# Performance work log

Measured on AMD Instinct MI355X. Metric: run time of the kernel, lower is better.

Reference implementation:

```python
import jax, jax.numpy as jnp
import numpy as np

B, L, H, HKV, D, HID, FFN = 32, 4096, 32, 2, 128, 4096, 13696
ROT = 64  # rotary_dim = kv_channels // 2 (GLM style)
EPS = 1e-5


def setup_inputs() -> dict:
    key = jax.random.key(0)
    ks = jax.random.split(key, 9)
    s = 0.02
    return {
        "hidden_states": jax.random.normal(ks[0], (B, HID), jnp.float32),
        "context_lens": jax.random.randint(ks[1], (B,), 1, L - 1, dtype=jnp.int32),
        "key_cache": jax.random.normal(ks[2], (B, L, HKV, D), jnp.float32),
        "value_cache": jax.random.normal(ks[3], (B, L, HKV, D), jnp.float32),
        "w_ln1": jnp.ones((HID,), jnp.float32),
        "w_ln2": jnp.ones((HID,), jnp.float32),
        "w_qkv": jax.random.normal(ks[4], (HID, H * D + 2 * HKV * D), jnp.float32) * s,
        "b_qkv": jax.random.normal(ks[5], (H * D + 2 * HKV * D,), jnp.float32) * s,
        "w_dense": jax.random.normal(ks[6], (H * D, HID), jnp.float32) * s,
        "w_h4h": jax.random.normal(ks[7], (HID, 2 * FFN), jnp.float32) * s,
        "w_4hh": jax.random.normal(ks[8], (FFN, HID), jnp.float32) * s,
    }


def rmsnorm(x, w):
    v = jnp.mean(x.astype(jnp.float32) ** 2, axis=-1, keepdims=True)
    return (w * (x * jax.lax.rsqrt(v + EPS))).astype(x.dtype)


def apply_rope(x, pos):
    # x: [B, heads, D]; GPT-J interleaved rotary on first ROT dims (glm=True)
    half = ROT // 2
    inv = 1.0 / (10000.0 ** (jnp.arange(half, dtype=jnp.float32) / half))
    f = pos.astype(jnp.float32)[:, None] * inv[None, :]          # [B, half]
    cos, sin = jnp.cos(f)[:, None, :], jnp.sin(f)[:, None, :]    # [B,1,half]
    xr, xp = x[..., :ROT], x[..., ROT:]
    x1, x2 = xr[..., 0::2], xr[..., 1::2]
    rot = jnp.stack([x1 * cos - x2 * sin, x2 * cos + x1 * sin], axis=-1).reshape(xr.shape)
    return jnp.concatenate([rot, xp], axis=-1)


def reference(hidden_states, context_lens, key_cache, value_cache,
              w_ln1, w_ln2, w_qkv, b_qkv, w_dense, w_h4h, w_4hh):
    # input RMSNorm
    ln1 = rmsnorm(hidden_states, w_ln1)
    # fused QKV projection (add_qkv_bias=True)
    qkv = ln1 @ w_qkv + b_qkv
    q, k, v = jnp.split(qkv, [H * D, H * D + HKV * D], axis=-1)
    q = apply_rope(q.reshape(B, H, D), context_lens)
    k = apply_rope(k.reshape(B, HKV, D), context_lens)
    v = v.reshape(B, HKV, D)
    # write new K/V into the paged cache at this token's slot
    kc = key_cache.at[jnp.arange(B), context_lens].set(k)
    vc = value_cache.at[jnp.arange(B), context_lens].set(v)
    # GQA attention: 32 q heads grouped over 2 kv heads
    qg = q.reshape(B, HKV, H // HKV, D)
    scores = jnp.einsum('bghd,blgd->bghl', qg, kc) * (D ** -0.5)
    mask = jnp.arange(L)[None, :] <= context_lens[:, None]       # [B, L]
    scores = jnp.where(mask[:, None, None, :], scores, -jnp.inf)
    p = jax.nn.softmax(scores, axis=-1)
    ctx = jnp.einsum('bghl,blgd->bghd', p, vc).reshape(B, H * D)
    attn_out = ctx @ w_dense                                     # add_bias_linear=False
    x = hidden_states + attn_out                                  # residual pre-LN
    ln2 = rmsnorm(x, w_ln2)
    g, u = jnp.split(ln2 @ w_h4h, 2, axis=-1)
    out = (jax.nn.silu(g) * u) @ w_4hh + x
    return out
```

## Files before the change

kernel.cpp:

```cpp
#include <hip/hip_runtime.h>
#include <hip/hip_bf16.h>

#define B_    32
#define L_    4096
#define H_    32
#define HKV_  2
#define GQ_   16
#define D_    128
#define HID_  4096
#define FFN_  13696
#define NQKV_ 4608
#define ROT_  64
#define EPS_  1e-5f

#define WAVE_POS_ 128
#define NSPLIT_   32

typedef __attribute__((ext_vector_type(8))) __bf16 bf16x8;
typedef __attribute__((ext_vector_type(4))) float  f32x4;

__global__ __launch_bounds__(256) void rmsnorm1_k(const float* __restrict__ x,
                                                  const float* __restrict__ w,
                                                  __bf16* __restrict__ out)
{
    int b = blockIdx.x;
    const float* row = x + (size_t)b * HID_;
    float vals[16];
    float ss = 0.f;
#pragma unroll
    for (int i = 0; i < 16; ++i) {
        vals[i] = row[threadIdx.x + i * 256];
        ss += vals[i] * vals[i];
    }
#pragma unroll
    for (int m = 1; m < 64; m <<= 1) ss += __shfl_xor(ss, m);
    __shared__ float wred[4];
    if ((threadIdx.x & 63) == 0) wred[threadIdx.x >> 6] = ss;
    __syncthreads();
    ss = wred[0] + wred[1] + wred[2] + wred[3];
    float rs = rsqrtf(ss / HID_ + EPS_);
#pragma unroll
    for (int i = 0; i < 16; ++i) {
        int idx = threadIdx.x + i * 256;
        out[(size_t)b * HID_ + idx] = (__bf16)(w[idx] * vals[i] * rs);
    }
}

template<int K, int N, int KSPLIT>
__global__ __launch_bounds__(256) void gemm16(const __bf16* __restrict__ A,
                                              const float* __restrict__ W,
                                              float* __restrict__ Cp)
{
    static_assert(K % 32 == 0, "K");
    constexpr int ksteps = K / 32;
    constexpr int nch    = KSPLIT * 4;
    const int lane = threadIdx.x & 63;
    const int wid  = threadIdx.x >> 6;
    const int n0   = blockIdx.x * 32;
    const int r    = lane & 15;
    const int g4   = lane >> 4;
    const int cid  = blockIdx.y * 4 + wid;
    const int s0   = (ksteps * cid) / nch;
    const int s1   = (ksteps * (cid + 1)) / nch;

    const int kk_b = lane >> 3;
    const int c4   = (lane & 7) * 4;

    __shared__ __bf16 tiles[4][32][40];
    __bf16 (*tile)[40] = tiles[wid];

    f32x4 acc00 = {0.f,0.f,0.f,0.f}, acc01 = acc00, acc10 = acc00, acc11 = acc00;
    const __bf16* a0p = A + (size_t)r * K;
    const __bf16* a1p = A + (size_t)(r + 16) * K;

    float4 pf[4];
    auto issue = [&](int s) {
        const float* wk = W + (size_t)(s * 32 + kk_b) * N + n0 + c4;
#pragma unroll
        for (int it = 0; it < 4; ++it)
            pf[it] = *(const float4*)(wk + (size_t)(it * 8) * N);
    };

    if (s0 < s1) issue(s0);
    for (int s = s0; s < s1; ++s) {
        float4 cur[4];
#pragma unroll
        for (int it = 0; it < 4; ++it) cur[it] = pf[it];
        if (s + 1 < s1) issue(s + 1);
#pragma unroll
        for (int it = 0; it < 4; ++it) {
            int kk = it * 8 + kk_b;
            tile[c4 + 0][kk] = (__bf16)cur[it].x;
            tile[c4 + 1][kk] = (__bf16)cur[it].y;
            tile[c4 + 2][kk] = (__bf16)cur[it].z;
            tile[c4 + 3][kk] = (__bf16)cur[it].w;
        }
        asm volatile("s_waitcnt lgkmcnt(0)" ::: "memory");
        __builtin_amdgcn_sched_barrier(0);
        bf16x8 b0  = *(const bf16x8*)&tile[r][g4 * 8];
        bf16x8 b1  = *(const bf16x8*)&tile[r + 16][g4 * 8];
        bf16x8 av0 = *(const bf16x8*)(a0p + s * 32 + g4 * 8);
        bf16x8 av1 = *(const bf16x8*)(a1p + s * 32 + g4 * 8);
        acc00 = __builtin_amdgcn_mfma_f32_16x16x32_bf16(av0, b0, acc00, 0, 0, 0);
        acc10 = __builtin_amdgcn_mfma_f32_16x16x32_bf16(av1, b0, acc10, 0, 0, 0);
        acc01 = __builtin_amdgcn_mfma_f32_16x16x32_bf16(av0, b1, acc01, 0, 0, 0);
        acc11 = __builtin_amdgcn_mfma_f32_16x16x32_bf16(av1, b1, acc11, 0, 0, 0);
        asm volatile("s_waitcnt lgkmcnt(0)" ::: "memory");
        __builtin_amdgcn_sched_barrier(0);
    }

    __shared__ float red[4][32][32];
#pragma unroll
    for (int i = 0; i < 4; ++i) {
        red[wid][g4 * 4 + i][r]           = acc00[i];
        red[wid][g4 * 4 + i][16 + r]      = acc01[i];
        red[wid][16 + g4 * 4 + i][r]      = acc10[i];
        red[wid][16 + g4 * 4 + i][16 + r] = acc11[i];
    }
    __syncthreads();
    for (int idx = threadIdx.x; idx < 1024; idx += 256) {
        int row = idx >> 5, col = idx & 31;
        float v = red[0][row][col] + red[1][row][col] + red[2][row][col] + red[3][row][col];
        Cp[((size_t)blockIdx.y * 32 + row) * N + n0 + col] = v;
    }
}

__global__ __launch_bounds__(256) void qkv_epi_k(const float* __restrict__ part,
                                                 const float* __restrict__ bias,
                                                 const int* __restrict__ ctxl,
                                                 __bf16* __restrict__ qbf,
                                                 float* __restrict__ knew,
                                                 float* __restrict__ vnew)
{
    __shared__ float rowv[NQKV_];
    __shared__ float cs[32], sn[32];
    int b = blockIdx.x;
    int pos = ctxl[b];
    if (threadIdx.x < 32) {
        int t = threadIdx.x;
        float inv = powf(10000.f, -(float)t * (1.0f / 32.0f));
        float f = (float)pos * inv;
        float sv, cv; sincosf(f, &sv, &cv);
        cs[t] = cv; sn[t] = sv;
    }
    for (int i = threadIdx.x; i < NQKV_; i += 256) {
        float v = bias[i];
#pragma unroll
        for (int p = 0; p < 4; ++p) v += part[((size_t)p * B_ + b) * NQKV_ + i];
        rowv[i] = v;
    }
    __syncthreads();
    const float qscale = 0.08838834764831845f;
    for (int i = threadIdx.x; i < HID_; i += 256) {
        int d = i & 127;
        float o;
        if (d < ROT_) {
            int t = d >> 1;
            float cv = cs[t], sv = sn[t];
            float x1 = rowv[i & ~1], x2 = rowv[i | 1];
            o = (d & 1) ? (x2 * cv + x1 * sv) : (x1 * cv - x2 * sv);
        } else o = rowv[i];
        qbf[(size_t)b * HID_ + i] = (__bf16)(o * qscale);
    }
    for (int i = threadIdx.x; i < HKV_ * D_; i += 256) {
        int d = i & 127;
        float o;
        if (d < ROT_) {
            int t = d >> 1;
            float cv = cs[t], sv = sn[t];
            float x1 = rowv[HID_ + (i & ~1)], x2 = rowv[HID_ + (i | 1)];
            o = (d & 1) ? (x2 * cv + x1 * sv) : (x1 * cv - x2 * sv);
        } else o = rowv[HID_ + i];
        knew[(size_t)b * HKV_ * D_ + i] = o;
        vnew[(size_t)b * HKV_ * D_ + i] = rowv[HID_ + HKV_ * D_ + i];
    }
}

__global__ __launch_bounds__(256) void attn_k(const float* __restrict__ kc,
                                              const float* __restrict__ vc,
                                              const float* __restrict__ knew,
                                              const float* __restrict__ vnew,
                                              const __bf16* __restrict__ qbf,
                                              const int* __restrict__ ctxl,
                                              float* __restrict__ part)
{
    const int bg  = blockIdx.x;
    const int b   = bg >> 1, g = bg & 1;
    const int wid = threadIdx.x >> 6;
    const int split = blockIdx.y * 4 + wid;
    const int ctx = ctxl[b];
    const int p0  = split * WAVE_POS_;
    __shared__ __bf16 plds_all[4][16][40];
    if (p0 > ctx) return;
    const int pend = min(p0 + WAVE_POS_ - 1, ctx);
    const int lane = threadIdx.x & 63;
    const int r = lane & 15, g4 = lane >> 4;

    bf16x8 qf[4];
    {
        const __bf16* qp = qbf + (size_t)b * HID_ + (g * GQ_ + r) * D_ + g4 * 8;
#pragma unroll
        for (int kk = 0; kk < 4; ++kk) qf[kk] = *(const bf16x8*)(qp + kk * 32);
    }
    f32x4 acc[8];
#pragma unroll
    for (int dt = 0; dt < 8; ++dt) acc[dt] = (f32x4){0.f,0.f,0.f,0.f};
    float m_run[4], l_run[4];
#pragma unroll
    for (int i = 0; i < 4; ++i) { m_run[i] = -1e30f; l_run[i] = 0.f; }

    auto plds = plds_all[wid];
    const float* kbase = kc + ((size_t)b * L_ * HKV_ + g) * D_;
    const float* vbase = vc + ((size_t)b * L_ * HKV_ + g) * D_;
    const float* knp = knew + (size_t)(b * HKV_ + g) * D_;
    const float* vnp = vnew + (size_t)(b * HKV_ + g) * D_;

    for (int pc = p0; pc <= pend; pc += 32) {
        f32x4 sf[2];
#pragma unroll
        for (int pt = 0; pt < 2; ++pt) {
            int pos = pc + pt * 16 + r;
            const float* krow = (pos == ctx) ? knp : kbase + (size_t)pos * (HKV_ * D_);
            f32x4 s = {0.f,0.f,0.f,0.f};
#pragma unroll
            for (int kk = 0; kk < 4; ++kk) {
                const float4* kp = (const float4*)(krow + kk * 32 + g4 * 8);
                float4 fa = kp[0], fb = kp[1];
                bf16x8 kf = { (__bf16)fa.x, (__bf16)fa.y, (__bf16)fa.z, (__bf16)fa.w,
                              (__bf16)fb.x, (__bf16)fb.y, (__bf16)fb.z, (__bf16)fb.w };
                s = __builtin_amdgcn_mfma_f32_16x16x32_bf16(qf[kk], kf, s, 0, 0, 0);
            }
            sf[pt] = s;
        }
#pragma unroll
        for (int pt = 0; pt < 2; ++pt) {
            int pos = pc + pt * 16 + r;
            if (pos > ctx) {
#pragma unroll
                for (int i = 0; i < 4; ++i) sf[pt][i] = -1e30f;
            }
        }
#pragma unroll
        for (int i = 0; i < 4; ++i) {
            float mv = fmaxf(sf[0][i], sf[1][i]);
            mv = fmaxf(mv, __shfl_xor(mv, 1));
            mv = fmaxf(mv, __shfl_xor(mv, 2));
            mv = fmaxf(mv, __shfl_xor(mv, 4));
            mv = fmaxf(mv, __shfl_xor(mv, 8));
            float mnew = fmaxf(m_run[i], mv);
            float sc = __expf(m_run[i] - mnew);
            l_run[i] *= sc;
            m_run[i] = mnew;
#pragma unroll
            for (int dt = 0; dt < 8; ++dt) acc[dt][i] *= sc;
        }
#pragma unroll
        for (int pt = 0; pt < 2; ++pt) {
#pragma unroll
            for (int i = 0; i < 4; ++i) {
                float e = __expf(sf[pt][i] - m_run[i]);
                l_run[i] += e;
                plds[g4 * 4 + i][pt * 16 + r] = (__bf16)e;
            }
        }
        asm volatile("s_waitcnt lgkmcnt(0)" ::: "memory");
        __builtin_amdgcn_sched_barrier(0);
        bf16x8 pa = *(const bf16x8*)&plds[r][g4 * 8];
        const float* vrows[8];
#pragma unroll
        for (int j = 0; j < 8; ++j) {
            int pos = pc + g4 * 8 + j;
            vrows[j] = (pos == ctx) ? vnp : vbase + (size_t)pos * (HKV_ * D_);
        }
#pragma unroll
        for (int dt = 0; dt < 8; ++dt) {
            bf16x8 vf;
#pragma unroll
            for (int j = 0; j < 8; ++j) vf[j] = (__bf16)vrows[j][dt * 16 + r];
            acc[dt] = __builtin_amdgcn_mfma_f32_16x16x32_bf16(pa, vf, acc[dt], 0, 0, 0);
        }
        asm volatile("s_waitcnt lgkmcnt(0)" ::: "memory");
        __builtin_amdgcn_sched_barrier(0);
    }
#pragma unroll
    for (int i = 0; i < 4; ++i) {
        float lv = l_run[i];
        lv += __shfl_xor(lv, 1);
        lv += __shfl_xor(lv, 2);
        lv += __shfl_xor(lv, 4);
        lv += __shfl_xor(lv, 8);
        l_run[i] = lv;
    }
    float* pb = part + ((size_t)bg * NSPLIT_ + split) * 16 * 130;
#pragma unroll
    for (int dt = 0; dt < 8; ++dt)
#pragma unroll
        for (int i = 0; i < 4; ++i)
            pb[(g4 * 4 + i) * 130 + dt * 16 + r] = acc[dt][i];
    if (r == 0) {
#pragma unroll
        for (int i = 0; i < 4; ++i) {
            pb[(g4 * 4 + i) * 130 + 128] = m_run[i];
            pb[(g4 * 4 + i) * 130 + 129] = l_run[i];
        }
    }
}

__global__ __launch_bounds__(256) void attn_comb_k(const float* __restrict__ part,
                                                   const int* __restrict__ ctxl,
                                                   __bf16* __restrict__ ctxb)
{
    int bg = blockIdx.x;
    int b = bg >> 1, g = bg & 1;
    int ctx = ctxl[b];
    int ns = ctx / WAVE_POS_ + 1;
    const float* pb = part + (size_t)bg * NSPLIT_ * 16 * 130;
    __shared__ float Wgt[NSPLIT_][16];
    __shared__ float Dn[16];
    int t = threadIdx.x;
    if (t < 16) {
        int h = t;
        float M = -1e30f;
        for (int s = 0; s < ns; ++s) M = fmaxf(M, pb[(s * 16 + h) * 130 + 128]);
        float den = 0.f;
        for (int s = 0; s < ns; ++s) {
            float w = __expf(pb[(s * 16 + h) * 130 + 128] - M);
            Wgt[s][h] = w;
            den += w * pb[(s * 16 + h) * 130 + 129];
        }
        Dn[h] = den;
    }
    __syncthreads();
    int h = t >> 4, d0 = (t & 15) * 8;
    float o[8];
#pragma unroll
    for (int j = 0; j < 8; ++j) o[j] = 0.f;
    for (int s = 0; s < ns; ++s) {
        float w = Wgt[s][h];
        const float* ap = pb + (s * 16 + h) * 130 + d0;
#pragma unroll
        for (int j = 0; j < 8; ++j) o[j] += w * ap[j];
    }
    float inv = 1.f / Dn[h];
#pragma unroll
    for (int j = 0; j < 8; ++j)
        ctxb[(size_t)b * HID_ + (g * GQ_ + h) * D_ + d0 + j] = (__bf16)(o[j] * inv);
}

__global__ __launch_bounds__(256) void dense_epi_k(const float* __restrict__ hidden,
                                                   const float* __restrict__ partd,
                                                   const float* __restrict__ wln2,
                                                   float* __restrict__ xout,
                                                   __bf16* __restrict__ a2)
{
    __shared__ float xr[HID_];
    int b = blockIdx.x;
    float ss = 0.f;
    for (int i = threadIdx.x; i < HID_; i += 256) {
        float v = hidden[(size_t)b * HID_ + i];
#pragma unroll
        for (int p = 0; p < 4; ++p) v += partd[((size_t)p * B_ + b) * HID_ + i];
        xr[i] = v;
        ss += v * v;
        xout[(size_t)b * HID_ + i] = v;
    }
#pragma unroll
    for (int m = 1; m < 64; m <<= 1) ss += __shfl_xor(ss, m);
    __shared__ float wred[4];
    if ((threadIdx.x & 63) == 0) wred[threadIdx.x >> 6] = ss;
    __syncthreads();
    ss = wred[0] + wred[1] + wred[2] + wred[3];
    float rs = rsqrtf(ss / HID_ + EPS_);
    for (int i = threadIdx.x; i < HID_; i += 256)
        a2[(size_t)b * HID_ + i] = (__bf16)(wln2[i] * xr[i] * rs);
}

__global__ __launch_bounds__(256) void act_k(const float* __restrict__ gu,
                                             __bf16* __restrict__ act)
{
    int i = blockIdx.x * 256 + threadIdx.x;
    int b = blockIdx.y;
    if (i < FFN_) {
        float gv = gu[(size_t)b * 2 * FFN_ + i];
        float uv = gu[(size_t)b * 2 * FFN_ + FFN_ + i];
        float s = gv / (1.f + __expf(-gv));
        act[(size_t)b * FFN_ + i] = (__bf16)(s * uv);
    }
}

__global__ __launch_bounds__(256) void out_epi_k(const float* __restrict__ x,
                                                 const float* __restrict__ part4,
                                                 float* __restrict__ out)
{
    int i = blockIdx.x * 256 + threadIdx.x;
    float v = x[i];
#pragma unroll
    for (int p = 0; p < 4; ++p) v += part4[(size_t)p * (B_ * HID_) + i];
    out[i] = v;
}

extern "C" void kernel_launch(void* const* d_in, const int* in_sizes, int n_in,
                              void* d_out, int out_size, void* d_ws, size_t ws_size,
                              hipStream_t stream)
{
    const float* hidden  = (const float*)d_in[0];
    const int*   ctxl    = (const int*)d_in[1];
    const float* kcache  = (const float*)d_in[2];
    const float* vcache  = (const float*)d_in[3];
    const float* w_ln1   = (const float*)d_in[4];
    const float* w_ln2   = (const float*)d_in[5];
    const float* w_qkv   = (const float*)d_in[6];
    const float* b_qkv   = (const float*)d_in[7];
    const float* w_dense = (const float*)d_in[8];
    const float* w_h4h   = (const float*)d_in[9];
    const float* w_4hh   = (const float*)d_in[10];
    float* out = (float*)d_out;

    char* ws = (char*)d_ws;
    size_t off = 0;
    auto alloc = [&](size_t bytes) -> void* {
        void* p = ws + off;
        off += (bytes + 255) & ~(size_t)255;
        return p;
    };
    __bf16* a0    = (__bf16*)alloc((size_t)B_ * HID_ * 2);
    float*  partq = (float*) alloc((size_t)4 * B_ * NQKV_ * 4);
    __bf16* qbf   = (__bf16*)alloc((size_t)B_ * HID_ * 2);
    float*  knew  = (float*) alloc((size_t)B_ * HKV_ * D_ * 4);
    float*  vnew  = (float*) alloc((size_t)B_ * HKV_ * D_ * 4);
    float*  apart = (float*) alloc((size_t)B_ * HKV_ * NSPLIT_ * 16 * 130 * 4);
    __bf16* ctxb  = (__bf16*)alloc((size_t)B_ * HID_ * 2);
    float*  partd = (float*) alloc((size_t)4 * B_ * HID_ * 4);
    float*  xbuf  = (float*) alloc((size_t)B_ * HID_ * 4);
    __bf16* a2    = (__bf16*)alloc((size_t)B_ * HID_ * 2);
    float*  gu    = (float*) alloc((size_t)B_ * 2 * FFN_ * 4);
    __bf16* actb  = (__bf16*)alloc((size_t)B_ * FFN_ * 2);
    float*  part4 = (float*) alloc((size_t)4 * B_ * HID_ * 4);
    (void)ws_size; (void)in_sizes; (void)n_in; (void)out_size;

    hipLaunchKernelGGL(rmsnorm1_k, dim3(B_), dim3(256), 0, stream, hidden, w_ln1, a0);
    hipLaunchKernelGGL((gemm16<HID_, NQKV_, 4>), dim3(NQKV_ / 32, 4), dim3(256), 0, stream, a0, w_qkv, partq);
    hipLaunchKernelGGL(qkv_epi_k, dim3(B_), dim3(256), 0, stream, partq, b_qkv, ctxl, qbf, knew, vnew);
    hipLaunchKernelGGL(attn_k, dim3(B_ * HKV_, NSPLIT_ / 4), dim3(256), 0, stream,
                       kcache, vcache, knew, vnew, qbf, ctxl, apart);
    hipLaunchKernelGGL(attn_comb_k, dim3(B_ * HKV_), dim3(256), 0, stream, apart, ctxl, ctxb);
    hipLaunchKernelGGL((gemm16<HID_, HID_, 4>), dim3(HID_ / 32, 4), dim3(256), 0, stream, ctxb, w_dense, partd);
    hipLaunchKernelGGL(dense_epi_k, dim3(B_), dim3(256), 0, stream, hidden, partd, w_ln2, xbuf, a2);
    hipLaunchKernelGGL((gemm16<HID_, 2 * FFN_, 1>), dim3(2 * FFN_ / 32, 1), dim3(256), 0, stream, a2, w_h4h, gu);
    hipLaunchKernelGGL(act_k, dim3((FFN_ + 255) / 256, B_), dim3(256), 0, stream, gu, actb);
    hipLaunchKernelGGL((gemm16<FFN_, HID_, 4>), dim3(HID_ / 32, 4), dim3(256), 0, stream, actb, w_4hh, part4);
    hipLaunchKernelGGL(out_epi_k, dim3(B_ * HID_ / 256), dim3(256), 0, stream, xbuf, part4, out);
}
```

Baseline: 300.5 us.

## Double-buffer GEMM weight prefetch and double split-K and attention splits

The gemm16 loop now processes two k-steps per iteration with two register prefetch buffers and two LDS tiles, so weight loads for step s+2 and s+3 are in flight while the current MFMAs run. Split-K is doubled for every projection GEMM (8 for QKV, dense and down, 2 for gate/up), with the epilogues summing the extra partials. Attention uses 64 splits of 64 positions each. These changes raise memory-level parallelism and CU occupancy on a weight-bandwidth-bound decode step. The cost is extra partial-sum traffic, more reduction work in the epilogues, and larger workspace buffers.

```diff
diff --git a/kernel.cpp b/kernel.cpp
--- a/kernel.cpp
+++ b/kernel.cpp
@@ -13,8 +13,8 @@
 #define ROT_  64
 #define EPS_  1e-5f
 
-#define WAVE_POS_ 128
-#define NSPLIT_   32
+#define WAVE_POS_ 64
+#define NSPLIT_   64
 
 typedef __attribute__((ext_vector_type(8))) __bf16 bf16x8;
 typedef __attribute__((ext_vector_type(4))) float  f32x4;
@@ -62,51 +62,79 @@
     const int cid  = blockIdx.y * 4 + wid;
     const int s0   = (ksteps * cid) / nch;
     const int s1   = (ksteps * (cid + 1)) / nch;
-
     const int kk_b = lane >> 3;
     const int c4   = (lane & 7) * 4;
 
-    __shared__ __bf16 tiles[4][32][40];
-    __bf16 (*tile)[40] = tiles[wid];
+    __shared__ __bf16 tA[4][32][34];
+    __shared__ __bf16 tB[4][32][34];
+    __bf16 (*ta)[34] = tA[wid];
+    __bf16 (*tb)[34] = tB[wid];
 
     f32x4 acc00 = {0.f,0.f,0.f,0.f}, acc01 = acc00, acc10 = acc00, acc11 = acc00;
     const __bf16* a0p = A + (size_t)r * K;
     const __bf16* a1p = A + (size_t)(r + 16) * K;
-
-    float4 pf[4];
-    auto issue = [&](int s) {
-        const float* wk = W + (size_t)(s * 32 + kk_b) * N + n0 + c4;
-#pragma unroll
-        for (int it = 0; it < 4; ++it)
-            pf[it] = *(const float4*)(wk + (size_t)(it * 8) * N);
+    const float*  wbase = W + n0 + c4;
+
+    float4 pf0[4], pf1[4];
+    auto issue0 = [&](int s) {
+        const float* p = wbase + (size_t)(s * 32 + kk_b) * N;
+#pragma unroll
+        for (int it = 0; it < 4; ++it) pf0[it] = *(const float4*)(p + (size_t)(it * 8) * N);
     };
-
-    if (s0 < s1) issue(s0);
-    for (int s = s0; s < s1; ++s) {
-        float4 cur[4];
-#pragma unroll
-        for (int it = 0; it < 4; ++it) cur[it] = pf[it];
-        if (s + 1 < s1) issue(s + 1);
+    auto issue1 = [&](int s) {
+        const float* p = wbase + (size_t)(s * 32 + kk_b) * N;
+#pragma unroll
+        for (int it = 0; it < 4; ++it) pf1[it] = *(const float4*)(p + (size_t)(it * 8) * N);
+    };
+    auto clampi = [&](int s) { return s < s1 ? s : s1 - 1; };
+
+    if (s0 < s1) {
+        issue0(s0);
+        issue1(clampi(s0 + 1));
+    }
+    for (int s = s0; s < s1; s += 2) {
+        bf16x8 av0 = *(const bf16x8*)(a0p + s * 32 + g4 * 8);
+        bf16x8 av1 = *(const bf16x8*)(a1p + s * 32 + g4 * 8);
 #pragma unroll
         for (int it = 0; it < 4; ++it) {
             int kk = it * 8 + kk_b;
-            tile[c4 + 0][kk] = (__bf16)cur[it].x;
-            tile[c4 + 1][kk] = (__bf16)cur[it].y;
-            tile[c4 + 2][kk] = (__bf16)cur[it].z;
-            tile[c4 + 3][kk] = (__bf16)cur[it].w;
-        }
+            ta[c4 + 0][kk] = (__bf16)pf0[it].x;
+            ta[c4 + 1][kk] = (__bf16)pf0[it].y;
+            ta[c4 + 2][kk] = (__bf16)pf0[it].z;
+            ta[c4 + 3][kk] = (__bf16)pf0[it].w;
+        }
+        issue0(clampi(s + 2));
         asm volatile("s_waitcnt lgkmcnt(0)" ::: "memory");
         __builtin_amdgcn_sched_barrier(0);
-        bf16x8 b0  = *(const bf16x8*)&tile[r][g4 * 8];
-        bf16x8 b1  = *(const bf16x8*)&tile[r + 16][g4 * 8];
-        bf16x8 av0 = *(const bf16x8*)(a0p + s * 32 + g4 * 8);
-        bf16x8 av1 = *(const bf16x8*)(a1p + s * 32 + g4 * 8);
-        acc00 = __builtin_amdgcn_mfma_f32_16x16x32_bf16(av0, b0, acc00, 0, 0, 0);
-        acc10 = __builtin_amdgcn_mfma_f32_16x16x32_bf16(av1, b0, acc10, 0, 0, 0);
-        acc01 = __builtin_amdgcn_mfma_f32_16x16x32_bf16(av0, b1, acc01, 0, 0, 0);
-        acc11 = __builtin_amdgcn_mfma_f32_16x16x32_bf16(av1, b1, acc11, 0, 0, 0);
-        asm volatile("s_waitcnt lgkmcnt(0)" ::: "memory");
-        __builtin_amdgcn_sched_barrier(0);
+        {
+            bf16x8 b0 = *(const bf16x8*)&ta[r][g4 * 8];
+            bf16x8 b1 = *(const bf16x8*)&ta[r + 16][g4 * 8];
+            acc00 = __builtin_amdgcn_mfma_f32_16x16x32_bf16(av0, b0, acc00, 0, 0, 0);
+            acc10 = __builtin_amdgcn_mfma_f32_16x16x32_bf16(av1, b0, acc10, 0, 0, 0);
+            acc01 = __builtin_amdgcn_mfma_f32_16x16x32_bf16(av0, b1, acc01, 0, 0, 0);
+            acc11 = __builtin_amdgcn_mfma_f32_16x16x32_bf16(av1, b1, acc11, 0, 0, 0);
+        }
+        if (s + 1 < s1) {
+            bf16x8 av2 = *(const bf16x8*)(a0p + (s + 1) * 32 + g4 * 8);
+            bf16x8 av3 = *(const bf16x8*)(a1p + (s + 1) * 32 + g4 * 8);
+#pragma unroll
+            for (int it = 0; it < 4; ++it) {
+                int kk = it * 8 + kk_b;
+                tb[c4 + 0][kk] = (__bf16)pf1[it].x;
+                tb[c4 + 1][kk] = (__bf16)pf1[it].y;
+                tb[c4 + 2][kk] = (__bf16)pf1[it].z;
+                tb[c4 + 3][kk] = (__bf16)pf1[it].w;
+            }
+            issue1(clampi(s + 3));
+            asm volatile("s_waitcnt lgkmcnt(0)" ::: "memory");
+            __builtin_amdgcn_sched_barrier(0);
+            bf16x8 b0 = *(const bf16x8*)&tb[r][g4 * 8];
+            bf16x8 b1 = *(const bf16x8*)&tb[r + 16][g4 * 8];
+            acc00 = __builtin_amdgcn_mfma_f32_16x16x32_bf16(av2, b0, acc00, 0, 0, 0);
+            acc10 = __builtin_amdgcn_mfma_f32_16x16x32_bf16(av3, b0, acc10, 0, 0, 0);
+            acc01 = __builtin_amdgcn_mfma_f32_16x16x32_bf16(av2, b1, acc01, 0, 0, 0);
+            acc11 = __builtin_amdgcn_mfma_f32_16x16x32_bf16(av3, b1, acc11, 0, 0, 0);
+        }
     }
 
     __shared__ float red[4][32][32];
@@ -146,7 +174,7 @@
     for (int i = threadIdx.x; i < NQKV_; i += 256) {
         float v = bias[i];
 #pragma unroll
-        for (int p = 0; p < 4; ++p) v += part[((size_t)p * B_ + b) * NQKV_ + i];
+        for (int p = 0; p < 8; ++p) v += part[((size_t)p * B_ + b) * NQKV_ + i];
         rowv[i] = v;
     }
     __syncthreads();
@@ -359,7 +387,7 @@
     for (int i = threadIdx.x; i < HID_; i += 256) {
         float v = hidden[(size_t)b * HID_ + i];
 #pragma unroll
-        for (int p = 0; p < 4; ++p) v += partd[((size_t)p * B_ + b) * HID_ + i];
+        for (int p = 0; p < 8; ++p) v += partd[((size_t)p * B_ + b) * HID_ + i];
         xr[i] = v;
         ss += v * v;
         xout[(size_t)b * HID_ + i] = v;
@@ -381,8 +409,10 @@
     int i = blockIdx.x * 256 + threadIdx.x;
     int b = blockIdx.y;
     if (i < FFN_) {
-        float gv = gu[(size_t)b * 2 * FFN_ + i];
-        float uv = gu[(size_t)b * 2 * FFN_ + FFN_ + i];
+        const float* g0 = gu + (size_t)b * 2 * FFN_;
+        const float* g1 = gu + ((size_t)B_ + b) * 2 * FFN_;
+        float gv = g0[i] + g1[i];
+        float uv = g0[FFN_ + i] + g1[FFN_ + i];
         float s = gv / (1.f + __expf(-gv));
         act[(size_t)b * FFN_ + i] = (__bf16)(s * uv);
     }
@@ -395,7 +425,7 @@
     int i = blockIdx.x * 256 + threadIdx.x;
     float v = x[i];
 #pragma unroll
-    for (int p = 0; p < 4; ++p) v += part4[(size_t)p * (B_ * HID_) + i];
+    for (int p = 0; p < 8; ++p) v += part4[(size_t)p * (B_ * HID_) + i];
     out[i] = v;
 }
 
@@ -424,30 +454,30 @@
         return p;
     };
     __bf16* a0    = (__bf16*)alloc((size_t)B_ * HID_ * 2);
-    float*  partq = (float*) alloc((size_t)4 * B_ * NQKV_ * 4);
+    float*  partq = (float*) alloc((size_t)8 * B_ * NQKV_ * 4);
     __bf16* qbf   = (__bf16*)alloc((size_t)B_ * HID_ * 2);
     float*  knew  = (float*) alloc((size_t)B_ * HKV_ * D_ * 4);
     float*  vnew  = (float*) alloc((size_t)B_ * HKV_ * D_ * 4);
     float*  apart = (float*) alloc((size_t)B_ * HKV_ * NSPLIT_ * 16 * 130 * 4);
     __bf16* ctxb  = (__bf16*)alloc((size_t)B_ * HID_ * 2);
-    float*  partd = (float*) alloc((size_t)4 * B_ * HID_ * 4);
+    float*  partd = (float*) alloc((size_t)8 * B_ * HID_ * 4);
     float*  xbuf  = (float*) alloc((size_t)B_ * HID_ * 4);
     __bf16* a2    = (__bf16*)alloc((size_t)B_ * HID_ * 2);
-    float*  gu    = (float*) alloc((size_t)B_ * 2 * FFN_ * 4);
+    float*  gu    = (float*) alloc((size_t)2 * B_ * 2 * FFN_ * 4);
     __bf16* actb  = (__bf16*)alloc((size_t)B_ * FFN_ * 2);
-    float*  part4 = (float*) alloc((size_t)4 * B_ * HID_ * 4);
+    float*  part4 = (float*) alloc((size_t)8 * B_ * HID_ * 4);
     (void)ws_size; (void)in_sizes; (void)n_in; (void)out_size;
 
     hipLaunchKernelGGL(rmsnorm1_k, dim3(B_), dim3(256), 0, stream, hidden, w_ln1, a0);
-    hipLaunchKernelGGL((gemm16<HID_, NQKV_, 4>), dim3(NQKV_ / 32, 4), dim3(256), 0, stream, a0, w_qkv, partq);
+    hipLaunchKernelGGL((gemm16<HID_, NQKV_, 8>), dim3(NQKV_ / 32, 8), dim3(256), 0, stream, a0, w_qkv, partq);
     hipLaunchKernelGGL(qkv_epi_k, dim3(B_), dim3(256), 0, stream, partq, b_qkv, ctxl, qbf, knew, vnew);
     hipLaunchKernelGGL(attn_k, dim3(B_ * HKV_, NSPLIT_ / 4), dim3(256), 0, stream,
                        kcache, vcache, knew, vnew, qbf, ctxl, apart);
     hipLaunchKernelGGL(attn_comb_k, dim3(B_ * HKV_), dim3(256), 0, stream, apart, ctxl, ctxb);
-    hipLaunchKernelGGL((gemm16<HID_, HID_, 4>), dim3(HID_ / 32, 4), dim3(256), 0, stream, ctxb, w_dense, partd);
+    hipLaunchKernelGGL((gemm16<HID_, HID_, 8>), dim3(HID_ / 32, 8), dim3(256), 0, stream, ctxb, w_dense, partd);
     hipLaunchKernelGGL(dense_epi_k, dim3(B_), dim3(256), 0, stream, hidden, partd, w_ln2, xbuf, a2);
-    hipLaunchKernelGGL((gemm16<HID_, 2 * FFN_, 1>), dim3(2 * FFN_ / 32, 1), dim3(256), 0, stream, a2, w_h4h, gu);
+    hipLaunchKernelGGL((gemm16<HID_, 2 * FFN_, 2>), dim3(2 * FFN_ / 32, 2), dim3(256), 0, stream, a2, w_h4h, gu);
     hipLaunchKernelGGL(act_k, dim3((FFN_ + 255) / 256, B_), dim3(256), 0, stream, gu, actb);
-    hipLaunchKernelGGL((gemm16<FFN_, HID_, 4>), dim3(HID_ / 32, 4), dim3(256), 0, stream, actb, w_4hh, part4);
+    hipLaunchKernelGGL((gemm16<FFN_, HID_, 8>), dim3(HID_ / 32, 8), dim3(256), 0, stream, actb, w_4hh, part4);
     hipLaunchKernelGGL(out_epi_k, dim3(B_ * HID_ / 256), dim3(256), 0, stream, xbuf, part4, out);
 }
```

Measured after the change: 322.6 us. 7.3% more time.
